# Kernel optimization log

Measured on AMD Instinct MI355X. Metric: run time of the kernel, lower is better.

## Reference

```python
import jax, jax.numpy as jnp
import numpy as np


def _lstm_scan(x_proj, Wh, b, c0, h0):
    """Run an LSTM over time. x_proj: [S, B, 4F] (inputs pre-projected by Wi).
    Flax OptimizedLSTMCell gate order: i, f, g, o."""
    def step(carry, xp):
        c, h = carry
        z = xp + h @ Wh + b                      # [B, 4F]
        i, f, g, o = jnp.split(z, 4, axis=-1)
        c = jax.nn.sigmoid(f) * c + jax.nn.sigmoid(i) * jnp.tanh(g)
        h = jax.nn.sigmoid(o) * jnp.tanh(c)
        return (c, h), h
    return jax.lax.scan(step, (c0, h0), x_proj)


def setup_inputs() -> dict:
    key = jax.random.key(0)
    ks = jax.random.split(key, 7)
    B, S, H, F = 16, 4096, 256, 256
    sH = 1.0 / np.sqrt(H)
    sF = 1.0 / np.sqrt(F)
    return {
        "inputs": jax.random.normal(ks[0], (B, S, H), jnp.float32),
        "Wi_fw": jax.random.normal(ks[1], (H, 4 * F), jnp.float32) * sH,
        "Wh_fw": jax.random.normal(ks[2], (F, 4 * F), jnp.float32) * sF,
        "b_fw": jnp.zeros((4 * F,), jnp.float32),
        "Wi_rv": jax.random.normal(ks[3], (H, 4 * F), jnp.float32) * sH,
        "Wh_rv": jax.random.normal(ks[4], (F, 4 * F), jnp.float32) * sF,
        "b_rv": jnp.zeros((4 * F,), jnp.float32),
    }


def reference(inputs, Wi_fw, Wh_fw, b_fw, Wi_rv, Wh_rv, b_rv):
    B, S, H = inputs.shape
    F = Wh_fw.shape[0]
    x = inputs.transpose(1, 0, 2)                       # [S, B, H] time-major
    zeros = jnp.zeros((B, F), inputs.dtype)

    # forward direction: pre-project all timesteps (one big GEMM), then scan
    xp_fw = jnp.einsum('sbh,hf->sbf', x, Wi_fw)         # [S, B, 4F]
    (c_fw, h_fw), hs_fw = _lstm_scan(xp_fw, Wh_fw, b_fw, zeros, zeros)

    # reverse direction: flax Bidirectional flips time, runs, flips back
    xp_rv = jnp.einsum('sbh,hf->sbf', x[::-1], Wi_rv)   # [S, B, 4F]
    (c_rv, h_rv), hs_rv = _lstm_scan(xp_rv, Wh_rv, b_rv, zeros, zeros)
    hs_rv = hs_rv[::-1]

    # merge_fn = _concatenate: [forward, reverse] along features
    output = jnp.concatenate([hs_fw, hs_rv], axis=-1).transpose(1, 0, 2)  # [B, S, 2F]
    return output, (c_fw, h_fw), (c_rv, h_rv)
```

## Files before the change

kernel.cpp:

```cpp
#include <hip/hip_runtime.h>

#define S_LEN 4096
#define BATCH 16
#define HID   256
#define GATE4 1024

typedef __bf16 bf16x8 __attribute__((ext_vector_type(8)));
typedef float  f32x4  __attribute__((ext_vector_type(4)));

union FragU {
    unsigned short u[8];
    bf16x8 v;
    uint4  q;
};

__device__ __forceinline__ unsigned short f2bf(float f) {
    unsigned u = __builtin_bit_cast(unsigned, f);
    u += 0x7fffu + ((u >> 16) & 1u);
    return (unsigned short)(u >> 16);
}
__device__ __forceinline__ float bf2f(unsigned short s) {
    unsigned u = ((unsigned)s) << 16;
    return __builtin_bit_cast(float, u);
}
__device__ __forceinline__ float sigmoid_f(float x) {
    return 1.f / (1.f + __expf(-x));
}
__device__ __forceinline__ float tanh_f(float x) {
    float e = __expf(2.f * x);
    return 1.f - 2.f / (e + 1.f);
}

__global__ void init_ctrl(unsigned int* ctrl, unsigned int* exch4) {
    int t = threadIdx.x;
    if (t < 128) ctrl[t] = (t == 16) ? 0xFFFFFFFFu : 0u;
    for (int i = t; i < 16384; i += 1024) exch4[i] = 0u;
}

__global__ __launch_bounds__(256, 2) void xp_gemm(
    const float* __restrict__ X,
    const float* __restrict__ Wi_fw, const float* __restrict__ b_fw,
    const float* __restrict__ Wi_rv, const float* __restrict__ b_rv,
    unsigned short* __restrict__ xp_fw, unsigned short* __restrict__ xp_rv)
{
    const int dir = blockIdx.z;
    const float* Wi   = dir ? Wi_rv : Wi_fw;
    const float* bias = dir ? b_rv  : b_fw;
    unsigned short* xp = dir ? xp_rv : xp_fw;

    __shared__ unsigned short As[64][40];
    __shared__ unsigned short Bs[64][40];

    const int tid  = threadIdx.x;
    const int lane = tid & 63;
    const int wid  = tid >> 6;
    const int quad = lane >> 4;
    const int l16  = lane & 15;
    const int wm = wid >> 1, wn = wid & 1;

    const int r0 = blockIdx.x * 64;
    const int n0 = blockIdx.y * 64;

    const int ai = tid & 63;
    const int ak = (tid >> 6) * 8;
    const int bk = tid >> 3;
    const int bj = (tid & 7) * 8;

    const int r  = r0 + ai;
    const int t  = r >> 4, bb = r & 15;
    const int t_eff = dir ? (S_LEN - 1 - t) : t;
    const float* Arow = X + ((size_t)bb * S_LEN + t_eff) * HID;

    f32x4 acc[2][2];
    #pragma unroll
    for (int i = 0; i < 2; ++i)
        #pragma unroll
        for (int j = 0; j < 2; ++j) { acc[i][j][0]=0.f; acc[i][j][1]=0.f; acc[i][j][2]=0.f; acc[i][j][3]=0.f; }

    for (int kb = 0; kb < HID / 32; ++kb) {
        {
            const float* p = Arow + kb * 32 + ak;
            float4 v0 = *(const float4*)p;
            float4 v1 = *(const float4*)(p + 4);
            FragU fu;
            fu.u[0]=f2bf(v0.x); fu.u[1]=f2bf(v0.y); fu.u[2]=f2bf(v0.z); fu.u[3]=f2bf(v0.w);
            fu.u[4]=f2bf(v1.x); fu.u[5]=f2bf(v1.y); fu.u[6]=f2bf(v1.z); fu.u[7]=f2bf(v1.w);
            *(uint4*)&As[ai][ak] = fu.q;
        }
        {
            const float* p = Wi + (size_t)(kb * 32 + bk) * GATE4 + n0 + bj;
            float4 v0 = *(const float4*)p;
            float4 v1 = *(const float4*)(p + 4);
            unsigned short tmp[8] = { f2bf(v0.x), f2bf(v0.y), f2bf(v0.z), f2bf(v0.w),
                                      f2bf(v1.x), f2bf(v1.y), f2bf(v1.z), f2bf(v1.w) };
            #pragma unroll
            for (int jj = 0; jj < 8; ++jj) Bs[bj + jj][bk] = tmp[jj];
        }
        __syncthreads();

        bf16x8 a0 = *(const bf16x8*)&As[wm * 32 + l16][quad * 8];
        bf16x8 a1 = *(const bf16x8*)&As[wm * 32 + 16 + l16][quad * 8];
        bf16x8 B0 = *(const bf16x8*)&Bs[wn * 32 + l16][quad * 8];
        bf16x8 B1 = *(const bf16x8*)&Bs[wn * 32 + 16 + l16][quad * 8];
        acc[0][0] = __builtin_amdgcn_mfma_f32_16x16x32_bf16(a0, B0, acc[0][0], 0, 0, 0);
        acc[0][1] = __builtin_amdgcn_mfma_f32_16x16x32_bf16(a0, B1, acc[0][1], 0, 0, 0);
        acc[1][0] = __builtin_amdgcn_mfma_f32_16x16x32_bf16(a1, B0, acc[1][0], 0, 0, 0);
        acc[1][1] = __builtin_amdgcn_mfma_f32_16x16x32_bf16(a1, B1, acc[1][1], 0, 0, 0);
        __syncthreads();
    }

    #pragma unroll
    for (int am = 0; am < 2; ++am)
        #pragma unroll
        for (int bn = 0; bn < 2; ++bn) {
            int ncol = n0 + wn * 32 + bn * 16 + l16;
            float bv = bias[ncol];
            #pragma unroll
            for (int rr = 0; rr < 4; ++rr) {
                int rrow = r0 + wm * 32 + am * 16 + quad * 4 + rr;
                float v = acc[am][bn][rr] + bv;
                xp[(size_t)rrow * GATE4 + ncol] = f2bf(v);
            }
        }
}

__global__ __launch_bounds__(512, 2) void lstm_rec(
    const float* __restrict__ Wh_fw, const float* __restrict__ Wh_rv,
    const unsigned short* __restrict__ xp_fw, const unsigned short* __restrict__ xp_rv,
    float* __restrict__ out,
    float* __restrict__ finals,
    char* __restrict__ exch,
    unsigned int* __restrict__ ctrl)
{
    const int tid  = threadIdx.x;
    __shared__ int role_s;

    if (tid == 0) {
        unsigned xcc;
        asm volatile("s_getreg_b32 %0, hwreg(HW_REG_XCC_ID)" : "=s"(xcc));
        xcc &= 7u;
        int role = -1;
        unsigned idx = atomicAdd(&ctrl[8u + xcc], 1u);
        if (idx < 4u) {
            if (idx == 3u) atomicCAS(&ctrl[16], 0xFFFFFFFFu, xcc);
            unsigned w;
            while ((w = __hip_atomic_fetch_add(&ctrl[16], 0u, __ATOMIC_RELAXED,
                                               __HIP_MEMORY_SCOPE_AGENT)) == 0xFFFFFFFFu)
                __builtin_amdgcn_s_sleep(2);
            if (w == xcc) role = (int)idx;
        }
        role_s = role;
    }
    __syncthreads();
    const int role = role_s;
    if (role < 0) return;

    const int dir  = role >> 1;
    const int half = role & 1;
    const float* Wh = dir ? Wh_rv : Wh_fw;
    const unsigned short* xp = dir ? xp_rv : xp_fw;

    const int lane = tid & 63;
    const int wid  = tid >> 6;
    const int quad = lane >> 4;
    const int l16  = lane & 15;

    const int fbase = half * 128 + wid * 16;
    const int floc  = wid * 16 + l16;
    const int po    = (1 - half) * 128;

    __shared__ unsigned short hbuf[2][16][264];

    for (int i = tid; i < 2 * 16 * 264; i += 512) (&hbuf[0][0][0])[i] = 0;

    bf16x8 Bfrag[4][8];
    #pragma unroll
    for (int g = 0; g < 4; ++g) {
        int col = g * 256 + fbase + l16;
        #pragma unroll
        for (int kt = 0; kt < 8; ++kt) {
            FragU fu;
            #pragma unroll
            for (int j = 0; j < 8; ++j) {
                int k = kt * 32 + quad * 8 + j;
                fu.u[j] = f2bf(Wh[(size_t)k * GATE4 + col]);
            }
            Bfrag[g][kt] = fu.v;
        }
    }

    float cst[4]  = {0.f, 0.f, 0.f, 0.f};
    float hval[4] = {0.f, 0.f, 0.f, 0.f};

    const size_t lanebase = (size_t)(quad * 4) * GATE4 + fbase + l16;

    unsigned long long* exA = (unsigned long long*)(exch
        + (size_t)(((dir * 2 + 0) * 2) + half) * 8192) + (size_t)tid * 2;
    unsigned long long* exB = (unsigned long long*)(exch
        + (size_t)(((dir * 2 + 1) * 2) + half) * 8192) + (size_t)tid * 2;
    const unsigned long long* pdA = (const unsigned long long*)(exch
        + (size_t)(((dir * 2 + 0) * 2) + (1 - half)) * 8192) + (size_t)tid * 2;
    const unsigned long long* pdB = (const unsigned long long*)(exch
        + (size_t)(((dir * 2 + 1) * 2) + (1 - half)) * 8192) + (size_t)tid * 2;

    unsigned short xpA[4][4], xpB[4][4];
    {
        const unsigned short* x0 = xp + lanebase;
        const unsigned short* x1 = xp + (size_t)BATCH * GATE4 + lanebase;
        #pragma unroll
        for (int g = 0; g < 4; ++g)
            #pragma unroll
            for (int rr = 0; rr < 4; ++rr) {
                xpA[g][rr] = x0[(size_t)rr * GATE4 + g * 256];
                xpB[g][rr] = x1[(size_t)rr * GATE4 + g * 256];
            }
    }

    __syncthreads();

    auto step = [&](int s, unsigned short (&xpc)[4][4],
                    unsigned long long* exm, const unsigned long long* pdm) {
        const int p = s & 1;
        const bool last = (s == S_LEN - 1);

        bf16x8 Afrag[8];
        #pragma unroll
        for (int kt = 0; kt < 8; ++kt)
            Afrag[kt] = *(const bf16x8*)&hbuf[p][l16][kt * 32 + quad * 8];

        f32x4 accg[4];
        #pragma unroll
        for (int g = 0; g < 4; ++g) { accg[g][0]=0.f; accg[g][1]=0.f; accg[g][2]=0.f; accg[g][3]=0.f; }
        #pragma unroll
        for (int kt = 0; kt < 8; ++kt) {
            accg[0] = __builtin_amdgcn_mfma_f32_16x16x32_bf16(Afrag[kt], Bfrag[0][kt], accg[0], 0, 0, 0);
            accg[1] = __builtin_amdgcn_mfma_f32_16x16x32_bf16(Afrag[kt], Bfrag[1][kt], accg[1], 0, 0, 0);
            accg[2] = __builtin_amdgcn_mfma_f32_16x16x32_bf16(Afrag[kt], Bfrag[2][kt], accg[2], 0, 0, 0);
            accg[3] = __builtin_amdgcn_mfma_f32_16x16x32_bf16(Afrag[kt], Bfrag[3][kt], accg[3], 0, 0, 0);
        }

        unsigned short hb[4];
        #pragma unroll
        for (int rr = 0; rr < 4; ++rr) {
            float zi = accg[0][rr] + bf2f(xpc[0][rr]);
            float zf = accg[1][rr] + bf2f(xpc[1][rr]);
            float zg = accg[2][rr] + bf2f(xpc[2][rr]);
            float zo = accg[3][rr] + bf2f(xpc[3][rr]);
            float ig = sigmoid_f(zi);
            float fg = sigmoid_f(zf);
            float gg = tanh_f(zg);
            float og = sigmoid_f(zo);
            float c  = fg * cst[rr] + ig * gg;
            cst[rr]  = c;
            float h  = og * tanh_f(c);
            hval[rr] = h;
            hb[rr]   = f2bf(h);
        }

        if (!last) {
            const unsigned long long tag = (unsigned long long)(unsigned)(s + 1) << 32;
            unsigned long long w0 = tag | (unsigned)hb[0] | ((unsigned)hb[1] << 16);
            unsigned long long w1 = tag | (unsigned)hb[2] | ((unsigned)hb[3] << 16);
            __hip_atomic_store(exm,     w0, __ATOMIC_RELAXED, __HIP_MEMORY_SCOPE_AGENT);
            __hip_atomic_store(exm + 1, w1, __ATOMIC_RELAXED, __HIP_MEMORY_SCOPE_AGENT);
        }

        #pragma unroll
        for (int rr = 0; rr < 4; ++rr)
            hbuf[p ^ 1][quad * 4 + rr][fbase + l16] = hb[rr];

        if (!last) {
            const unsigned tag = (unsigned)(s + 1);
            unsigned long long w0, w1;
            do {
                w0 = __hip_atomic_load(pdm,     __ATOMIC_RELAXED, __HIP_MEMORY_SCOPE_AGENT);
                w1 = __hip_atomic_load(pdm + 1, __ATOMIC_RELAXED, __HIP_MEMORY_SCOPE_AGENT);
            } while ((unsigned)(w0 >> 32) != tag || (unsigned)(w1 >> 32) != tag);

            hbuf[p ^ 1][quad * 4 + 0][po + floc] = (unsigned short)(w0);
            hbuf[p ^ 1][quad * 4 + 1][po + floc] = (unsigned short)(w0 >> 16);
            hbuf[p ^ 1][quad * 4 + 2][po + floc] = (unsigned short)(w1);
            hbuf[p ^ 1][quad * 4 + 3][po + floc] = (unsigned short)(w1 >> 16);
        }

        {
            int t_orig = dir ? (S_LEN - 1 - s) : s;
            float* ob = out + (size_t)t_orig * 512 + dir * 256 + fbase + l16;
            #pragma unroll
            for (int rr = 0; rr < 4; ++rr)
                ob[(size_t)(quad * 4 + rr) * S_LEN * 512] = hval[rr];
        }
        if (s + 2 < S_LEN) {
            const unsigned short* xr = xp + (size_t)(s + 2) * (BATCH * GATE4) + lanebase;
            #pragma unroll
            for (int g = 0; g < 4; ++g)
                #pragma unroll
                for (int rr = 0; rr < 4; ++rr)
                    xpc[g][rr] = xr[(size_t)rr * GATE4 + g * 256];
        }

        if (!last) {
            asm volatile("s_waitcnt lgkmcnt(0)" ::: "memory");
            __builtin_amdgcn_s_barrier();
        }
    };

    for (int s2 = 0; s2 < S_LEN; s2 += 2) {
        step(s2,     xpA, exA, pdA);
        step(s2 + 1, xpB, exB, pdB);
    }

    {
        float* cdst = finals + (dir ? 8192 : 0);
        float* hdst = cdst + 4096;
        #pragma unroll
        for (int rr = 0; rr < 4; ++rr) {
            int m = quad * 4 + rr;
            int f = fbase + l16;
            cdst[m * 256 + f] = cst[rr];
            hdst[m * 256 + f] = hval[rr];
        }
    }
}

extern "C" void kernel_launch(void* const* d_in, const int* in_sizes, int n_in,
                              void* d_out, int out_size, void* d_ws, size_t ws_size,
                              hipStream_t stream)
{
    const float* X     = (const float*)d_in[0];
    const float* Wi_fw = (const float*)d_in[1];
    const float* Wh_fw = (const float*)d_in[2];
    const float* b_fw  = (const float*)d_in[3];
    const float* Wi_rv = (const float*)d_in[4];
    const float* Wh_rv = (const float*)d_in[5];
    const float* b_rv  = (const float*)d_in[6];

    float* out    = (float*)d_out;
    float* finals = out + (size_t)BATCH * S_LEN * 512;

    char* ws = (char*)d_ws;
    unsigned short* xp_fw = (unsigned short*)ws;
    unsigned short* xp_rv = (unsigned short*)(ws + 134217728ull);
    char*           exch  = ws + 268435456ull;
    unsigned int*   ctrl  = (unsigned int*)(ws + 268435456ull + 65536ull);

    init_ctrl<<<1, 1024, 0, stream>>>(ctrl, (unsigned int*)exch);

    dim3 g(65536 / 64, 1024 / 64, 2);
    xp_gemm<<<g, 256, 0, stream>>>(X, Wi_fw, b_fw, Wi_rv, b_rv, xp_fw, xp_rv);

    lstm_rec<<<64, 512, 0, stream>>>(Wh_fw, Wh_rv, xp_fw, xp_rv, out, finals, exch, ctrl);
}
```

Measured before the change: 12.02 ms.

## Split recurrent matmul into local and peer halves to overlap exchange latency

Each step's h@Wh product is split by K into the half produced locally and the half received from the peer block. The local-half MFMAs run right after the block writes its own h to shared memory, before it polls for the peer's data, and the peer-half MFMAs run after the exchange completes. This hides part of the cross-block spin-wait behind useful matrix work. The cost is an extra block barrier per step, and the accumulator now lives across step boundaries.

```diff
diff --git a/kernel.cpp b/kernel.cpp
--- a/kernel.cpp
+++ b/kernel.cpp
@@ -168,10 +168,10 @@
     const int fbase = half * 128 + wid * 16;
     const int floc  = wid * 16 + l16;
     const int po    = (1 - half) * 128;
+    const int ko    = half * 4;
+    const int kp    = (1 - half) * 4;
 
     __shared__ unsigned short hbuf[2][16][264];
-
-    for (int i = tid; i < 2 * 16 * 264; i += 512) (&hbuf[0][0][0])[i] = 0;
 
     bf16x8 Bfrag[4][8];
     #pragma unroll
@@ -216,28 +216,14 @@
             }
     }
 
-    __syncthreads();
+    f32x4 accg[4];
+    #pragma unroll
+    for (int g = 0; g < 4; ++g) { accg[g][0]=0.f; accg[g][1]=0.f; accg[g][2]=0.f; accg[g][3]=0.f; }
 
     auto step = [&](int s, unsigned short (&xpc)[4][4],
                     unsigned long long* exm, const unsigned long long* pdm) {
-        const int p = s & 1;
+        const int q = s & 1;
         const bool last = (s == S_LEN - 1);
-
-        bf16x8 Afrag[8];
-        #pragma unroll
-        for (int kt = 0; kt < 8; ++kt)
-            Afrag[kt] = *(const bf16x8*)&hbuf[p][l16][kt * 32 + quad * 8];
-
-        f32x4 accg[4];
-        #pragma unroll
-        for (int g = 0; g < 4; ++g) { accg[g][0]=0.f; accg[g][1]=0.f; accg[g][2]=0.f; accg[g][3]=0.f; }
-        #pragma unroll
-        for (int kt = 0; kt < 8; ++kt) {
-            accg[0] = __builtin_amdgcn_mfma_f32_16x16x32_bf16(Afrag[kt], Bfrag[0][kt], accg[0], 0, 0, 0);
-            accg[1] = __builtin_amdgcn_mfma_f32_16x16x32_bf16(Afrag[kt], Bfrag[1][kt], accg[1], 0, 0, 0);
-            accg[2] = __builtin_amdgcn_mfma_f32_16x16x32_bf16(Afrag[kt], Bfrag[2][kt], accg[2], 0, 0, 0);
-            accg[3] = __builtin_amdgcn_mfma_f32_16x16x32_bf16(Afrag[kt], Bfrag[3][kt], accg[3], 0, 0, 0);
-        }
 
         unsigned short hb[4];
         #pragma unroll
@@ -258,50 +244,82 @@
         }
 
         if (!last) {
-            const unsigned long long tag = (unsigned long long)(unsigned)(s + 1) << 32;
-            unsigned long long w0 = tag | (unsigned)hb[0] | ((unsigned)hb[1] << 16);
-            unsigned long long w1 = tag | (unsigned)hb[2] | ((unsigned)hb[3] << 16);
-            __hip_atomic_store(exm,     w0, __ATOMIC_RELAXED, __HIP_MEMORY_SCOPE_AGENT);
-            __hip_atomic_store(exm + 1, w1, __ATOMIC_RELAXED, __HIP_MEMORY_SCOPE_AGENT);
-        }
-
-        #pragma unroll
-        for (int rr = 0; rr < 4; ++rr)
-            hbuf[p ^ 1][quad * 4 + rr][fbase + l16] = hb[rr];
-
-        if (!last) {
-            const unsigned tag = (unsigned)(s + 1);
+            const unsigned long long tg = (unsigned long long)(unsigned)(s + 1) << 32;
+            unsigned long long w0p = tg | (unsigned)hb[0] | ((unsigned)hb[1] << 16);
+            unsigned long long w1p = tg | (unsigned)hb[2] | ((unsigned)hb[3] << 16);
+            __hip_atomic_store(exm,     w0p, __ATOMIC_RELAXED, __HIP_MEMORY_SCOPE_AGENT);
+            __hip_atomic_store(exm + 1, w1p, __ATOMIC_RELAXED, __HIP_MEMORY_SCOPE_AGENT);
+
+            #pragma unroll
+            for (int rr = 0; rr < 4; ++rr)
+                hbuf[q][quad * 4 + rr][fbase + l16] = hb[rr];
+            asm volatile("s_waitcnt lgkmcnt(0)" ::: "memory");
+            __builtin_amdgcn_s_barrier();
+
+            bf16x8 Afrag[4];
+            #pragma unroll
+            for (int kt = 0; kt < 4; ++kt)
+                Afrag[kt] = *(const bf16x8*)&hbuf[q][l16][(ko + kt) * 32 + quad * 8];
+            #pragma unroll
+            for (int g = 0; g < 4; ++g) { accg[g][0]=0.f; accg[g][1]=0.f; accg[g][2]=0.f; accg[g][3]=0.f; }
+            #pragma unroll
+            for (int kt = 0; kt < 4; ++kt) {
+                accg[0] = __builtin_amdgcn_mfma_f32_16x16x32_bf16(Afrag[kt], Bfrag[0][ko + kt], accg[0], 0, 0, 0);
+                accg[1] = __builtin_amdgcn_mfma_f32_16x16x32_bf16(Afrag[kt], Bfrag[1][ko + kt], accg[1], 0, 0, 0);
+                accg[2] = __builtin_amdgcn_mfma_f32_16x16x32_bf16(Afrag[kt], Bfrag[2][ko + kt], accg[2], 0, 0, 0);
+                accg[3] = __builtin_amdgcn_mfma_f32_16x16x32_bf16(Afrag[kt], Bfrag[3][ko + kt], accg[3], 0, 0, 0);
+            }
+            __builtin_amdgcn_sched_barrier(0);
+
+            const unsigned tagv = (unsigned)(s + 1);
             unsigned long long w0, w1;
             do {
                 w0 = __hip_atomic_load(pdm,     __ATOMIC_RELAXED, __HIP_MEMORY_SCOPE_AGENT);
                 w1 = __hip_atomic_load(pdm + 1, __ATOMIC_RELAXED, __HIP_MEMORY_SCOPE_AGENT);
-            } while ((unsigned)(w0 >> 32) != tag || (unsigned)(w1 >> 32) != tag);
-
-            hbuf[p ^ 1][quad * 4 + 0][po + floc] = (unsigned short)(w0);
-            hbuf[p ^ 1][quad * 4 + 1][po + floc] = (unsigned short)(w0 >> 16);
-            hbuf[p ^ 1][quad * 4 + 2][po + floc] = (unsigned short)(w1);
-            hbuf[p ^ 1][quad * 4 + 3][po + floc] = (unsigned short)(w1 >> 16);
-        }
-
-        {
+            } while ((unsigned)(w0 >> 32) != tagv || (unsigned)(w1 >> 32) != tagv);
+
+            if (s + 2 < S_LEN) {
+                const unsigned short* xr = xp + (size_t)(s + 2) * (BATCH * GATE4) + lanebase;
+                #pragma unroll
+                for (int g = 0; g < 4; ++g)
+                    #pragma unroll
+                    for (int rr = 0; rr < 4; ++rr)
+                        xpc[g][rr] = xr[(size_t)rr * GATE4 + g * 256];
+            }
+
+            hbuf[q][quad * 4 + 0][po + floc] = (unsigned short)(w0);
+            hbuf[q][quad * 4 + 1][po + floc] = (unsigned short)(w0 >> 16);
+            hbuf[q][quad * 4 + 2][po + floc] = (unsigned short)(w1);
+            hbuf[q][quad * 4 + 3][po + floc] = (unsigned short)(w1 >> 16);
+
+            {
+                int t_orig = dir ? (S_LEN - 1 - s) : s;
+                float* ob = out + (size_t)t_orig * 512 + dir * 256 + fbase + l16;
+                #pragma unroll
+                for (int rr = 0; rr < 4; ++rr)
+                    ob[(size_t)(quad * 4 + rr) * S_LEN * 512] = hval[rr];
+            }
+
+            asm volatile("s_waitcnt lgkmcnt(0)" ::: "memory");
+            __builtin_amdgcn_s_barrier();
+
+            bf16x8 Pfrag[4];
+            #pragma unroll
+            for (int kt = 0; kt < 4; ++kt)
+                Pfrag[kt] = *(const bf16x8*)&hbuf[q][l16][(kp + kt) * 32 + quad * 8];
+            #pragma unroll
+            for (int kt = 0; kt < 4; ++kt) {
+                accg[0] = __builtin_amdgcn_mfma_f32_16x16x32_bf16(Pfrag[kt], Bfrag[0][kp + kt], accg[0], 0, 0, 0);
+                accg[1] = __builtin_amdgcn_mfma_f32_16x16x32_bf16(Pfrag[kt], Bfrag[1][kp + kt], accg[1], 0, 0, 0);
+                accg[2] = __builtin_amdgcn_mfma_f32_16x16x32_bf16(Pfrag[kt], Bfrag[2][kp + kt], accg[2], 0, 0, 0);
+                accg[3] = __builtin_amdgcn_mfma_f32_16x16x32_bf16(Pfrag[kt], Bfrag[3][kp + kt], accg[3], 0, 0, 0);
+            }
+        } else {
             int t_orig = dir ? (S_LEN - 1 - s) : s;
             float* ob = out + (size_t)t_orig * 512 + dir * 256 + fbase + l16;
             #pragma unroll
             for (int rr = 0; rr < 4; ++rr)
                 ob[(size_t)(quad * 4 + rr) * S_LEN * 512] = hval[rr];
-        }
-        if (s + 2 < S_LEN) {
-            const unsigned short* xr = xp + (size_t)(s + 2) * (BATCH * GATE4) + lanebase;
-            #pragma unroll
-            for (int g = 0; g < 4; ++g)
-                #pragma unroll
-                for (int rr = 0; rr < 4; ++rr)
-                    xpc[g][rr] = xr[(size_t)rr * GATE4 + g * 256];
-        }
-
-        if (!last) {
-            asm volatile("s_waitcnt lgkmcnt(0)" ::: "memory");
-            __builtin_amdgcn_s_barrier();
         }
     };
 
```

After: 38.78 ms. 223% more time.
